# Performance work log

Hardware: AMD Instinct MI355X
Metric: run time of the kernel (lower is better)

The kernel has to match this reference:

```python
import jax, jax.numpy as jnp
import numpy as np

K = 1024
D = 256
BETA = 0.25


def setup_inputs() -> dict:
    key = jax.random.key(0)
    k1, k2 = jax.random.split(key)
    latents = jax.random.normal(k1, (32, D, 32, 32), dtype=jnp.float32)
    # nn.Embedding init: uniform(-1/K, 1/K)
    embedding = jax.random.uniform(k2, (K, D), dtype=jnp.float32,
                                   minval=-1.0 / K, maxval=1.0 / K)
    return {"latents": latents, "embedding": embedding}


def reference(latents, embedding):
    # latents: [B, D, H, W] -> [B, H, W, D]
    x = jnp.transpose(latents, (0, 2, 3, 1))
    input_shape = x.shape
    flat = x.reshape(-1, D)  # [N, D]

    # squared-L2 distances to codebook: [N, K]
    distances = (jnp.sum(flat ** 2, axis=1, keepdims=True)
                 + jnp.sum(embedding ** 2, axis=1)
                 - 2.0 * flat @ embedding.T)
    encoding_indices = jnp.argmin(distances, axis=1)  # [N]

    # one-hot encodings (returned output); quantize via direct gather
    encodings = jax.nn.one_hot(encoding_indices, K, dtype=latents.dtype)  # [N, K]
    quantized = embedding[encoding_indices].reshape(input_shape)  # [B, H, W, D]

    e_latent_loss = jnp.mean((jax.lax.stop_gradient(quantized) - x) ** 2)
    q_latent_loss = jnp.mean((quantized - jax.lax.stop_gradient(x)) ** 2)
    loss = q_latent_loss + BETA * e_latent_loss

    # straight-through estimator
    quantized_st = x + jax.lax.stop_gradient(quantized - x)

    avg_probs = jnp.mean(encodings, axis=0)  # [K]
    perplexity = jnp.exp(-jnp.sum(avg_probs * jnp.log(avg_probs + 1e-10)))

    return (loss,
            jnp.transpose(quantized_st, (0, 3, 1, 2)),  # [B, D, H, W]
            perplexity,
            encodings)
```

## Files before the change

kernel.cpp:

```cpp
#include <hip/hip_runtime.h>
#include <stdint.h>
#include <math.h>

typedef float  f32x4 __attribute__((ext_vector_type(4)));
typedef float  f32x2 __attribute__((ext_vector_type(2)));
typedef short  s16x8 __attribute__((ext_vector_type(8)));

#define KC   1024
#define DD   256
#define NR   32768

#define WS_HIST   0
#define WS_ACC    4096
#define WS_E2     8192
#define WS_IDX    12288
#define WS_PANEL  143360
#define WS_PART   671744

#define ENC_OFF   8388610ULL

#define A_OFF   0
#define B_OFF   32768
#define E2_OFF  65536
#define SMEM_SZ 67584

#define GLD16(gp, lp) __builtin_amdgcn_global_load_lds(                      \
    (const __attribute__((address_space(1))) uint32_t*)(gp),                 \
    (__attribute__((address_space(3))) uint32_t*)(lp), 16, 0, 0)

#define WAITVM(N) asm volatile("s_waitcnt vmcnt(" #N ")" ::: "memory")
#define PHASEBAR() do { __builtin_amdgcn_s_barrier();                        \
                        __builtin_amdgcn_sched_barrier(0); } while (0)

__device__ __forceinline__ short f2bf(float f) {
    uint32_t u = __builtin_bit_cast(uint32_t, f);
    uint32_t r = (u + 0x7FFFu + ((u >> 16) & 1u)) >> 16;
    return (short)r;
}

__global__ void k_prep(const float* __restrict__ emb, char* __restrict__ ws) {
    int tid = threadIdx.x;
    if (blockIdx.x == 0) {
        uint32_t* hist = (uint32_t*)(ws + WS_HIST);
        #pragma unroll
        for (int j = 0; j < 4; j++) hist[tid * 4 + j] = 0u;
        if (tid < 2) ((float*)(ws + WS_ACC))[tid] = 0.f;
    }
    int wid = tid >> 6, lane = tid & 63;
    int code = blockIdx.x * 4 + wid;
    const float* row = emb + (size_t)code * DD;
    f32x4 v = *(const f32x4*)(row + lane * 4);
    uint32_t lo = (uint32_t)(uint16_t)f2bf(v.x) | ((uint32_t)(uint16_t)f2bf(v.y) << 16);
    uint32_t hi = (uint32_t)(uint16_t)f2bf(v.z) | ((uint32_t)(uint16_t)f2bf(v.w) << 16);
    uint32_t* dst = (uint32_t*)((short*)(ws + WS_PANEL) + (size_t)code * DD + lane * 4);
    __builtin_nontemporal_store(lo, dst);
    __builtin_nontemporal_store(hi, dst + 1);
    float ss = v.x * v.x + v.y * v.y + v.z * v.z + v.w * v.w;
    #pragma unroll
    for (int off = 1; off < 64; off <<= 1) ss += __shfl_xor(ss, off);
    if (lane == 0)
        __builtin_nontemporal_store(ss + 1.0f, (float*)(ws + WS_E2) + code);
}

__global__ __launch_bounds__(256, 2) void k_argmin(const float* __restrict__ latents,
                                                   char* __restrict__ ws) {
    const char*  panelb = (const char*)(ws + WS_PANEL);
    const float* e2g    = (const float*)(ws + WS_E2);
    float*       acc    = (float*)(ws + WS_ACC);

    __shared__ __align__(16) char smem[SMEM_SZ];

    int t      = threadIdx.x;
    int lane   = t & 63;
    int wid    = t >> 6;
    int g      = lane >> 4, r16 = lane & 15;
    int rowgrp = blockIdx.x & 255;
    int chalf  = blockIdx.x >> 8;
    int nbase  = rowgrp * 128;
    int b      = nbase >> 10;
    int hwbase = nbase & 1023;
    int phase  = rowgrp & 31;
    const char* pbase = panelb + (size_t)chalf * 262144;

    if (t < 128) {
        f32x4 ev = *(const f32x4*)(e2g + chalf * 512 + t * 4);
        *(f32x4*)(smem + E2_OFF + t * 16) = ev;
    }

    float xs = 0.f;
    s16x8 af[2][8];
    int rg = (t & 15) * 4;
    int dp = (t >> 4) * 2;

    #pragma unroll
    for (int h = 0; h < 2; h++) {
        const float* base = latents + (size_t)b * 262144 + hwbase + h * 64 + rg;
        #pragma unroll
        for (int i = 0; i < 8; i++) {
            int d = dp + i * 32;
            f32x4 v0 = *(const f32x4*)(base + (size_t)d * 1024);
            f32x4 v1 = *(const f32x4*)(base + (size_t)(d + 1) * 1024);
            xs += v0.x*v0.x + v0.y*v0.y + v0.z*v0.z + v0.w*v0.w;
            xs += v1.x*v1.x + v1.y*v1.y + v1.z*v1.z + v1.w*v1.w;
            int qb = d >> 3;
            #pragma unroll
            for (int q = 0; q < 4; q++) {
                int slot = rg + q;
                uint32_t pk = (uint32_t)(uint16_t)f2bf(v0[q])
                            | ((uint32_t)(uint16_t)f2bf(v1[q]) << 16);
                int quad = qb ^ (slot & 7) ^ ((slot >> 3) & 7);
                *(uint32_t*)(smem + A_OFF + slot * 512 + quad * 16 + (d & 6) * 2) = pk;
            }
        }
        __syncthreads();
        if ((wid >> 1) == h) {
            int slotbase = (wid & 1) * 32;
            #pragma unroll
            for (int rt = 0; rt < 2; rt++) {
                #pragma unroll
                for (int kt = 0; kt < 8; kt++) {
                    int slot = slotbase + rt * 16 + r16;
                    int quad = (kt * 4 + g) ^ (slot & 7) ^ ((slot >> 3) & 7);
                    af[rt][kt] = *(const s16x8*)(smem + A_OFF + slot * 512 + quad * 16);
                }
            }
        }
        __syncthreads();
    }
    if (chalf == 0) {
        #pragma unroll
        for (int off = 1; off < 64; off <<= 1) xs += __shfl_xor(xs, off);
        if (lane == 0) atomicAdd(acc + 0, xs);
    }

    float vmin[2][4];
    #pragma unroll
    for (int rt = 0; rt < 2; rt++)
        #pragma unroll
        for (int j = 0; j < 4; j++) vmin[rt][j] = 3.4e38f;

    const float* E2l = (const float*)(smem + E2_OFF);
    int codeglob = chalf * 512;

    auto stage = [&](int c) {
        const char* srcc = pbase + (size_t)c * 8192;
        char* dstb = smem + B_OFF + (size_t)(c & 3) * 8192;
        #pragma unroll
        for (int i = 0; i < 2; i++) {
            uint32_t off = i * 4096 + wid * 1024;
            uint32_t so  = off + lane * 16;
            uint32_t ssw = so ^ (((so >> 9) & 7u) << 4);
            GLD16(srcc + ssw, dstb + off);
        }
    };
    auto compute = [&](int c) {
        int cbase = c * 16;
        float e2c = E2l[cbase + r16];
        uint32_t mycode = (uint32_t)(codeglob + cbase + r16);
        const char* Bc = smem + B_OFF + (size_t)(c & 3) * 8192;
        s16x8 bf[8];
        #pragma unroll
        for (int kt = 0; kt < 8; kt++) {
            uint32_t byte = (uint32_t)(r16 * 512)
                          + (((uint32_t)(kt * 64 + g * 16)) ^ (((uint32_t)(r16 & 7)) << 4));
            bf[kt] = *(const s16x8*)(Bc + byte);
        }
        #pragma unroll
        for (int rt = 0; rt < 2; rt++) {
            f32x4 a4 = {0.f, 0.f, 0.f, 0.f};
            #pragma unroll
            for (int kt = 0; kt < 8; kt++)
                a4 = __builtin_amdgcn_mfma_f32_16x16x32_bf16(af[rt][kt], bf[kt], a4, 0, 0, 0);
            #pragma unroll
            for (int j = 0; j < 4; j++) {
                float s = __builtin_fmaf(a4[j], -2.f, e2c);
                uint32_t pk = (__builtin_bit_cast(uint32_t, s) & 0xFFFFFC00u) | mycode;
                float sp = __builtin_bit_cast(float, pk);
                vmin[rt][j] = fminf(vmin[rt][j], sp);
            }
        }
    };

    stage(phase); stage((phase + 1) & 31); stage((phase + 2) & 31);
    #pragma unroll 1
    for (int c = 0; c < 29; ++c) {
        WAITVM(4);
        PHASEBAR();
        compute((c + phase) & 31);
        stage((c + 3 + phase) & 31);
    }
    WAITVM(4); PHASEBAR(); compute((29 + phase) & 31);
    WAITVM(2); PHASEBAR(); compute((30 + phase) & 31);
    WAITVM(0); PHASEBAR(); compute((31 + phase) & 31);

    uint32_t* part = (uint32_t*)(ws + WS_PART) + (size_t)chalf * NR;
    #pragma unroll
    for (int rt = 0; rt < 2; rt++) {
        #pragma unroll
        for (int j = 0; j < 4; j++) {
            float s = vmin[rt][j];
            #pragma unroll
            for (int off = 1; off < 16; off <<= 1)
                s = fminf(s, __shfl_xor(s, off));
            if (r16 == 0) {
                int n = nbase + wid * 32 + rt * 16 + g * 4 + j;
                part[n] = __builtin_bit_cast(uint32_t, s);
            }
        }
    }
}

__global__ void k_comb(char* __restrict__ ws) {
    const uint32_t* part = (const uint32_t*)(ws + WS_PART);
    uint32_t* hist = (uint32_t*)(ws + WS_HIST);
    float*    acc  = (float*)(ws + WS_ACC);
    int*      idxo = (int*)(ws + WS_IDX);
    int n = blockIdx.x * 256 + threadIdx.x;
    uint32_t p0 = part[n];
    uint32_t p1 = part[NR + n];
    uint32_t p = (p1 < p0) ? p1 : p0;
    int  ii = (int)(p & 1023u);
    float s = __builtin_bit_cast(float, p & 0xFFFFFC00u) - 1.0f;
    idxo[n] = ii;
    atomicAdd(hist + ii, 1u);
    #pragma unroll
    for (int off = 1; off < 64; off <<= 1) s += __shfl_xor(s, off);
    if ((threadIdx.x & 63) == 0) atomicAdd(acc + 1, s);
}

__global__ void k_quant(const float* __restrict__ emb, const char* __restrict__ ws,
                        float* __restrict__ out) {
    const int* idx = (const int*)(ws + WS_IDX);
    int tid = threadIdx.x;
    int dg  = blockIdx.x & 63;
    int hwt = (blockIdx.x >> 6) & 3;
    int b   = blockIdx.x >> 8;
    int hw  = hwt * 256 + tid;
    int n   = b * 1024 + hw;
    int code = idx[n];
    f32x4 v = *(const f32x4*)(emb + (size_t)code * 256 + dg * 4);
    float* dst = out + 1 + (size_t)b * 262144 + (size_t)dg * 4096 + hw;
    dst[0] = v.x; dst[1024] = v.y; dst[2048] = v.z; dst[3072] = v.w;
}

__global__ void k_onehot(const char* __restrict__ ws, float* __restrict__ out) {
    const int* idx = (const int*)(ws + WS_IDX);
    __shared__ int lidx[8];
    int tid = threadIdx.x;
    int rbase = blockIdx.x * 8;
    if (tid < 8) lidx[tid] = idx[rbase + tid];
    __syncthreads();
    f32x2* enc = (f32x2*)(out + ENC_OFF);
    #pragma unroll
    for (int j = 0; j < 16; j++) {
        int linear = j * 256 + tid;
        int rl = linear >> 9, c2 = linear & 511;
        int id = lidx[rl];
        f32x2 v;
        v.x = (2 * c2     == id) ? 1.f : 0.f;
        v.y = (2 * c2 + 1 == id) ? 1.f : 0.f;
        enc[(size_t)(rbase + rl) * 512 + c2] = v;
    }
}

__global__ void k_final(const char* __restrict__ ws, float* __restrict__ out) {
    __shared__ float red[256];
    const uint32_t* hist = (const uint32_t*)(ws + WS_HIST);
    const float*    acc  = (const float*)(ws + WS_ACC);
    int tid = threadIdx.x;
    float part = 0.f;
    #pragma unroll
    for (int j = 0; j < 4; j++) {
        float p = (float)hist[tid * 4 + j] * (1.f / 32768.f);
        part += p * logf(p + 1e-10f);
    }
    red[tid] = part;
    __syncthreads();
    for (int s = 128; s > 0; s >>= 1) {
        if (tid < s) red[tid] += red[tid + s];
        __syncthreads();
    }
    if (tid == 0) {
        out[8388609] = expf(-red[0]);
        out[0] = 1.25f * (acc[0] + acc[1]) * (1.f / 8388608.f);
    }
}

extern "C" void kernel_launch(void* const* d_in, const int* in_sizes, int n_in,
                              void* d_out, int out_size, void* d_ws, size_t ws_size,
                              hipStream_t stream) {
    const float* latents = (const float*)d_in[0];
    const float* emb     = (const float*)d_in[1];
    float* out = (float*)d_out;
    char*  ws  = (char*)d_ws;

    hipLaunchKernelGGL(k_prep,   dim3(256),  dim3(256), 0, stream, emb, ws);
    hipLaunchKernelGGL(k_argmin, dim3(512),  dim3(256), 0, stream, latents, ws);
    hipLaunchKernelGGL(k_comb,   dim3(128),  dim3(256), 0, stream, ws);
    hipLaunchKernelGGL(k_quant,  dim3(8192), dim3(256), 0, stream, emb, ws, out);
    hipLaunchKernelGGL(k_onehot, dim3(4096), dim3(256), 0, stream, ws, out);
    hipLaunchKernelGGL(k_final,  dim3(1),    dim3(256), 0, stream, ws, out);
}
```

Baseline: 89.94 us.

## Zero one-hot output inside argmin grid and scatter ones in combine kernel

Removes the separate one-hot kernel. Extra blocks appended to the argmin launch zero-fill the 128 MB encodings buffer with nontemporal stores, so that memory-bound write can overlap the compute-bound distance search. The combine kernel then writes a single 1.0 per row. This trades a dependent kernel launch for heavier argmin blocks that compete for CU slots and bandwidth, and the result relies on the zeroing blocks finishing before the combine kernel runs, which stream ordering guarantees.

Result: slower. 98.15 us (+9.1%).

```diff
diff --git a/kernel.cpp b/kernel.cpp
--- a/kernel.cpp
+++ b/kernel.cpp
@@ -63,19 +63,31 @@
 }
 
 __global__ __launch_bounds__(256, 2) void k_argmin(const float* __restrict__ latents,
-                                                   char* __restrict__ ws) {
+                                                   char* __restrict__ ws,
+                                                   float* __restrict__ out) {
+    int t = threadIdx.x;
+
+    if (blockIdx.x >= 512) {
+        int wb = blockIdx.x - 512;
+        f32x2* dst = (f32x2*)(out + ENC_OFF) + (size_t)wb * 32768 + t;
+        f32x2 z = {0.f, 0.f};
+        #pragma unroll 8
+        for (int j = 0; j < 128; j++)
+            __builtin_nontemporal_store(z, dst + j * 256);
+        return;
+    }
+
     const char*  panelb = (const char*)(ws + WS_PANEL);
     const float* e2g    = (const float*)(ws + WS_E2);
     float*       acc    = (float*)(ws + WS_ACC);
 
     __shared__ __align__(16) char smem[SMEM_SZ];
 
-    int t      = threadIdx.x;
     int lane   = t & 63;
     int wid    = t >> 6;
     int g      = lane >> 4, r16 = lane & 15;
     int rowgrp = blockIdx.x & 255;
-    int chalf  = blockIdx.x >> 8;
+    int chalf  = (blockIdx.x >> 8) & 1;
     int nbase  = rowgrp * 128;
     int b      = nbase >> 10;
     int hwbase = nbase & 1023;
@@ -210,7 +222,7 @@
     }
 }
 
-__global__ void k_comb(char* __restrict__ ws) {
+__global__ void k_comb(char* __restrict__ ws, float* __restrict__ out) {
     const uint32_t* part = (const uint32_t*)(ws + WS_PART);
     uint32_t* hist = (uint32_t*)(ws + WS_HIST);
     float*    acc  = (float*)(ws + WS_ACC);
@@ -222,6 +234,7 @@
     int  ii = (int)(p & 1023u);
     float s = __builtin_bit_cast(float, p & 0xFFFFFC00u) - 1.0f;
     idxo[n] = ii;
+    out[ENC_OFF + (size_t)n * 1024 + ii] = 1.f;
     atomicAdd(hist + ii, 1u);
     #pragma unroll
     for (int off = 1; off < 64; off <<= 1) s += __shfl_xor(s, off);
@@ -243,26 +256,6 @@
     dst[0] = v.x; dst[1024] = v.y; dst[2048] = v.z; dst[3072] = v.w;
 }
 
-__global__ void k_onehot(const char* __restrict__ ws, float* __restrict__ out) {
-    const int* idx = (const int*)(ws + WS_IDX);
-    __shared__ int lidx[8];
-    int tid = threadIdx.x;
-    int rbase = blockIdx.x * 8;
-    if (tid < 8) lidx[tid] = idx[rbase + tid];
-    __syncthreads();
-    f32x2* enc = (f32x2*)(out + ENC_OFF);
-    #pragma unroll
-    for (int j = 0; j < 16; j++) {
-        int linear = j * 256 + tid;
-        int rl = linear >> 9, c2 = linear & 511;
-        int id = lidx[rl];
-        f32x2 v;
-        v.x = (2 * c2     == id) ? 1.f : 0.f;
-        v.y = (2 * c2 + 1 == id) ? 1.f : 0.f;
-        enc[(size_t)(rbase + rl) * 512 + c2] = v;
-    }
-}
-
 __global__ void k_final(const char* __restrict__ ws, float* __restrict__ out) {
     __shared__ float red[256];
     const uint32_t* hist = (const uint32_t*)(ws + WS_HIST);
@@ -295,9 +288,8 @@
     char*  ws  = (char*)d_ws;
 
     hipLaunchKernelGGL(k_prep,   dim3(256),  dim3(256), 0, stream, emb, ws);
-    hipLaunchKernelGGL(k_argmin, dim3(512),  dim3(256), 0, stream, latents, ws);
-    hipLaunchKernelGGL(k_comb,   dim3(128),  dim3(256), 0, stream, ws);
+    hipLaunchKernelGGL(k_argmin, dim3(1024), dim3(256), 0, stream, latents, ws, out);
+    hipLaunchKernelGGL(k_comb,   dim3(128),  dim3(256), 0, stream, ws, out);
     hipLaunchKernelGGL(k_quant,  dim3(8192), dim3(256), 0, stream, emb, ws, out);
-    hipLaunchKernelGGL(k_onehot, dim3(4096), dim3(256), 0, stream, ws, out);
     hipLaunchKernelGGL(k_final,  dim3(1),    dim3(256), 0, stream, ws, out);
 }
```

## Convert codebook to bf16 inside argmin kernel instead of a prebuilt panel

Applied to the files above, without the earlier changes.

The prep kernel no longer writes a bf16 codebook panel to the workspace. The argmin kernel now loads fp32 embedding rows into registers, converts them to bf16, and writes them into a double-buffered LDS tile. This replaces the 4-deep async global-to-LDS pipeline with a register-staged prefetch and a full barrier every chunk. The aim is to drop the panel write/read traffic and shrink LDS use, at the cost of twice the global read bytes per chunk, conversion ALU work inside the loop, and a shallower pipeline.

Result: slower. 95.82 us (+6.5%).

```diff
diff --git a/kernel.cpp b/kernel.cpp
--- a/kernel.cpp
+++ b/kernel.cpp
@@ -5,6 +5,7 @@
 typedef float  f32x4 __attribute__((ext_vector_type(4)));
 typedef float  f32x2 __attribute__((ext_vector_type(2)));
 typedef short  s16x8 __attribute__((ext_vector_type(8)));
+typedef unsigned int u32x4 __attribute__((ext_vector_type(4)));
 
 #define KC   1024
 #define DD   256
@@ -14,29 +15,25 @@
 #define WS_ACC    4096
 #define WS_E2     8192
 #define WS_IDX    12288
-#define WS_PANEL  143360
-#define WS_PART   671744
+#define WS_PART   143360
 
 #define ENC_OFF   8388610ULL
 
 #define A_OFF   0
 #define B_OFF   32768
-#define E2_OFF  65536
-#define SMEM_SZ 67584
-
-#define GLD16(gp, lp) __builtin_amdgcn_global_load_lds(                      \
-    (const __attribute__((address_space(1))) uint32_t*)(gp),                 \
-    (__attribute__((address_space(3))) uint32_t*)(lp), 16, 0, 0)
+#define E2_OFF  49152
+#define SMEM_SZ 51200
 
 #define WAITVM(N) asm volatile("s_waitcnt vmcnt(" #N ")" ::: "memory")
-#define PHASEBAR() do { __builtin_amdgcn_s_barrier();                        \
-                        __builtin_amdgcn_sched_barrier(0); } while (0)
 
 __device__ __forceinline__ short f2bf(float f) {
     uint32_t u = __builtin_bit_cast(uint32_t, f);
     uint32_t r = (u + 0x7FFFu + ((u >> 16) & 1u)) >> 16;
     return (short)r;
 }
+__device__ __forceinline__ uint32_t pkbf(float a, float b) {
+    return (uint32_t)(uint16_t)f2bf(a) | ((uint32_t)(uint16_t)f2bf(b) << 16);
+}
 
 __global__ void k_prep(const float* __restrict__ emb, char* __restrict__ ws) {
     int tid = threadIdx.x;
@@ -50,11 +47,6 @@
     int code = blockIdx.x * 4 + wid;
     const float* row = emb + (size_t)code * DD;
     f32x4 v = *(const f32x4*)(row + lane * 4);
-    uint32_t lo = (uint32_t)(uint16_t)f2bf(v.x) | ((uint32_t)(uint16_t)f2bf(v.y) << 16);
-    uint32_t hi = (uint32_t)(uint16_t)f2bf(v.z) | ((uint32_t)(uint16_t)f2bf(v.w) << 16);
-    uint32_t* dst = (uint32_t*)((short*)(ws + WS_PANEL) + (size_t)code * DD + lane * 4);
-    __builtin_nontemporal_store(lo, dst);
-    __builtin_nontemporal_store(hi, dst + 1);
     float ss = v.x * v.x + v.y * v.y + v.z * v.z + v.w * v.w;
     #pragma unroll
     for (int off = 1; off < 64; off <<= 1) ss += __shfl_xor(ss, off);
@@ -63,10 +55,10 @@
 }
 
 __global__ __launch_bounds__(256, 2) void k_argmin(const float* __restrict__ latents,
+                                                   const float* __restrict__ emb,
                                                    char* __restrict__ ws) {
-    const char*  panelb = (const char*)(ws + WS_PANEL);
-    const float* e2g    = (const float*)(ws + WS_E2);
-    float*       acc    = (float*)(ws + WS_ACC);
+    const float* e2g = (const float*)(ws + WS_E2);
+    float*       acc = (float*)(ws + WS_ACC);
 
     __shared__ __align__(16) char smem[SMEM_SZ];
 
@@ -80,7 +72,6 @@
     int b      = nbase >> 10;
     int hwbase = nbase & 1023;
     int phase  = rowgrp & 31;
-    const char* pbase = panelb + (size_t)chalf * 262144;
 
     if (t < 128) {
         f32x4 ev = *(const f32x4*)(e2g + chalf * 512 + t * 4);
@@ -106,8 +97,7 @@
             #pragma unroll
             for (int q = 0; q < 4; q++) {
                 int slot = rg + q;
-                uint32_t pk = (uint32_t)(uint16_t)f2bf(v0[q])
-                            | ((uint32_t)(uint16_t)f2bf(v1[q]) << 16);
+                uint32_t pk = pkbf(v0[q], v1[q]);
                 int quad = qb ^ (slot & 7) ^ ((slot >> 3) & 7);
                 *(uint32_t*)(smem + A_OFF + slot * 512 + quad * 16 + (d & 6) * 2) = pk;
             }
@@ -142,22 +132,35 @@
     const float* E2l = (const float*)(smem + E2_OFF);
     int codeglob = chalf * 512;
 
-    auto stage = [&](int c) {
-        const char* srcc = pbase + (size_t)c * 8192;
-        char* dstb = smem + B_OFF + (size_t)(c & 3) * 8192;
-        #pragma unroll
-        for (int i = 0; i < 2; i++) {
-            uint32_t off = i * 4096 + wid * 1024;
-            uint32_t so  = off + lane * 16;
-            uint32_t ssw = so ^ (((so >> 9) & 7u) << 4);
-            GLD16(srcc + ssw, dstb + off);
-        }
+    int srow = t >> 4;
+    int sd0  = (t & 15) * 16;
+    const float* esrc0 = emb + (size_t)(codeglob + srow) * 256 + sd0;
+    uint32_t wbase = (uint32_t)(srow * 512);
+    uint32_t wsw   = ((uint32_t)(srow & 7)) << 4;
+    uint32_t wq0   = (uint32_t)((t & 15) * 2) * 16;
+    char* wdst0 = smem + B_OFF;
+
+    f32x4 sreg[4];
+    auto loadB = [&](int cc) {
+        const float* src = esrc0 + (size_t)cc * 4096;
+        #pragma unroll
+        for (int i = 0; i < 4; i++) sreg[i] = *(const f32x4*)(src + i * 4);
     };
-    auto compute = [&](int c) {
-        int cbase = c * 16;
+    auto writeB = [&](int par) {
+        char* dstb = wdst0 + par * 8192;
+        u32x4 w0, w1;
+        w0[0] = pkbf(sreg[0][0], sreg[0][1]); w0[1] = pkbf(sreg[0][2], sreg[0][3]);
+        w0[2] = pkbf(sreg[1][0], sreg[1][1]); w0[3] = pkbf(sreg[1][2], sreg[1][3]);
+        w1[0] = pkbf(sreg[2][0], sreg[2][1]); w1[1] = pkbf(sreg[2][2], sreg[2][3]);
+        w1[2] = pkbf(sreg[3][0], sreg[3][1]); w1[3] = pkbf(sreg[3][2], sreg[3][3]);
+        *(u32x4*)(dstb + wbase + (wq0 ^ wsw))        = w0;
+        *(u32x4*)(dstb + wbase + ((wq0 + 16) ^ wsw)) = w1;
+    };
+    auto compute = [&](int cc) {
+        int cbase = cc * 16;
         float e2c = E2l[cbase + r16];
         uint32_t mycode = (uint32_t)(codeglob + cbase + r16);
-        const char* Bc = smem + B_OFF + (size_t)(c & 3) * 8192;
+        const char* Bc = wdst0 + (cc & 1) * 8192;
         s16x8 bf[8];
         #pragma unroll
         for (int kt = 0; kt < 8; kt++) {
@@ -181,17 +184,21 @@
         }
     };
 
-    stage(phase); stage((phase + 1) & 31); stage((phase + 2) & 31);
+    {
+        int cc0 = phase;
+        loadB(cc0);
+        writeB(cc0 & 1);
+    }
+    __syncthreads();
     #pragma unroll 1
-    for (int c = 0; c < 29; ++c) {
-        WAITVM(4);
-        PHASEBAR();
-        compute((c + phase) & 31);
-        stage((c + 3 + phase) & 31);
-    }
-    WAITVM(4); PHASEBAR(); compute((29 + phase) & 31);
-    WAITVM(2); PHASEBAR(); compute((30 + phase) & 31);
-    WAITVM(0); PHASEBAR(); compute((31 + phase) & 31);
+    for (int c = 0; c < 32; ++c) {
+        int cc  = (c + phase) & 31;
+        int ccn = (c + 1 + phase) & 31;
+        if (c < 31) loadB(ccn);
+        compute(cc);
+        if (c < 31) writeB(ccn & 1);
+        __syncthreads();
+    }
 
     uint32_t* part = (uint32_t*)(ws + WS_PART) + (size_t)chalf * NR;
     #pragma unroll
@@ -295,7 +302,7 @@
     char*  ws  = (char*)d_ws;
 
     hipLaunchKernelGGL(k_prep,   dim3(256),  dim3(256), 0, stream, emb, ws);
-    hipLaunchKernelGGL(k_argmin, dim3(512),  dim3(256), 0, stream, latents, ws);
+    hipLaunchKernelGGL(k_argmin, dim3(512),  dim3(256), 0, stream, latents, emb, ws);
     hipLaunchKernelGGL(k_comb,   dim3(128),  dim3(256), 0, stream, ws);
     hipLaunchKernelGGL(k_quant,  dim3(8192), dim3(256), 0, stream, emb, ws, out);
     hipLaunchKernelGGL(k_onehot, dim3(4096), dim3(256), 0, stream, ws, out);
```
